# Kernel optimization log

Measured on AMD Instinct MI355X. Metric: run time of the kernel, lower is better.

## Reference

```python
import jax, jax.numpy as jnp
import numpy as np

DIM = 512
N_HEADS = 8
HEAD_DIM = DIM // N_HEADS


def rope_pos(T, head_dim, dtype=jnp.float32):
    inv_freq = 1.0 / (10000.0 ** (jnp.arange(0, head_dim, 2, dtype=jnp.float32) / head_dim))
    t = jnp.arange(T, dtype=jnp.float32)
    freqs = jnp.einsum('i,j->ij', t, inv_freq)            # [T, head_dim/2]
    return jnp.concatenate([freqs, freqs], axis=-1).astype(dtype)  # [T, head_dim]


def rotate_half(x):
    x1, x2 = jnp.split(x, 2, axis=-1)
    return jnp.concatenate([-x2, x1], axis=-1)


def apply_rope(pos, t):
    # pos: [T, hd] -> broadcast to [1,1,T,hd]; t: [B,H,T,hd]
    pos = pos[None, None, :, :]
    return t * jnp.cos(pos) + rotate_half(t) * jnp.sin(pos)


def setup_inputs() -> dict:
    key = jax.random.key(0)
    ks = jax.random.split(key, 6)
    B, T = 4, 2048
    x = jax.random.normal(ks[0], (B, T, DIM), dtype=jnp.float32)
    mask = jnp.zeros((B, T), dtype=jnp.float32)  # additive mask
    s = 1.0 / np.sqrt(DIM)
    qkv_w = jax.random.normal(ks[1], (3 * DIM, DIM), dtype=jnp.float32) * s
    qkv_b = jnp.zeros((3 * DIM,), dtype=jnp.float32)
    proj_w = jax.random.normal(ks[2], (DIM, DIM), dtype=jnp.float32) * s
    proj_b = jnp.zeros((DIM,), dtype=jnp.float32)
    return {"x": x, "mask": mask, "qkv_w": qkv_w, "qkv_b": qkv_b,
            "proj_w": proj_w, "proj_b": proj_b}


def reference(x, mask, qkv_w, qkv_b, proj_w, proj_b):
    B, T, C = x.shape
    qkv = x @ qkv_w.T + qkv_b                       # [B,T,3C]
    qkv = qkv.reshape(B, T, 3, N_HEADS, HEAD_DIM)
    q, k, v = qkv[:, :, 0], qkv[:, :, 1], qkv[:, :, 2]  # [B,T,H,hd]
    q = q.transpose(0, 2, 1, 3)                     # [B,H,T,hd]
    k = k.transpose(0, 2, 1, 3)
    v = v.transpose(0, 2, 1, 3)
    pos = rope_pos(T, HEAD_DIM, x.dtype)
    q = apply_rope(pos, q)
    k = apply_rope(pos, k)
    scores = jnp.einsum('bhqd,bhkd->bhqk', q, k) * (1.0 / np.sqrt(HEAD_DIM))
    scores = scores + mask[:, None, None, :]        # 2D mask -> [B,1,1,T]
    probs = jax.nn.softmax(scores.astype(jnp.float32), axis=-1).astype(x.dtype)
    # dropout is identity in eval mode
    out = jnp.einsum('bhqk,bhkd->bhqd', probs, v)   # [B,H,T,hd]
    out = out.transpose(0, 2, 1, 3).reshape(B, T, C)
    return out @ proj_w.T + proj_b
```

## Files before the change

### kernel.cpp

```cpp
#include <hip/hip_runtime.h>
#include <math.h>


typedef __attribute__((ext_vector_type(8))) short bf16x8;
typedef __attribute__((ext_vector_type(4))) float floatx4;

#define LOG2E 1.44269504088896f

__device__ __forceinline__ unsigned short f2bf(float f) {
  unsigned int u = __float_as_uint(f);
  u += 0x7fffu + ((u >> 16) & 1u);
  return (unsigned short)(u >> 16);
}

__device__ __forceinline__ unsigned int cvtpk_bf16(float a, float b) {
  unsigned int r;
  asm("v_cvt_pk_bf16_f32 %0, %1, %2" : "=v"(r) : "v"(a), "v"(b));
  return r;
}

__device__ __forceinline__ void gld_lds16(unsigned short* lds, const unsigned short* g) {
  __builtin_amdgcn_global_load_lds(
      (const __attribute__((address_space(1))) unsigned int*)g,
      (__attribute__((address_space(3))) unsigned int*)lds, 16, 0, 0);
}

__global__ __launch_bounds__(256) void prep_kernel(
    const float* __restrict__ x, const float* __restrict__ wq, const float* __restrict__ wp,
    unsigned short* __restrict__ xb, unsigned short* __restrict__ wqb,
    unsigned short* __restrict__ wpb, float* __restrict__ cosT, float* __restrict__ sinT) {
  int i = blockIdx.x * 256 + threadIdx.x;
  if (i < 655360) {
    int base = i * 8;
    const float* src;
    unsigned short* dst;
    int j;
    if (base < 4194304)      { src = x;  dst = xb;  j = base; }
    else if (base < 4980736) { src = wq; dst = wqb; j = base - 4194304; }
    else                     { src = wp; dst = wpb; j = base - 4980736; }
    float4 a = *(const float4*)(src + j);
    float4 b = *(const float4*)(src + j + 4);
    uint4 r;
    r.x = cvtpk_bf16(a.x, a.y);
    r.y = cvtpk_bf16(a.z, a.w);
    r.z = cvtpk_bf16(b.x, b.y);
    r.w = cvtpk_bf16(b.z, b.w);
    *(uint4*)(dst + j) = r;
  } else if (i < 720896) {
    int j = i - 655360;
    int t = j >> 5, f = j & 31;
    double fr = (double)t * pow(10000.0, -(double)f / 32.0);
    cosT[j] = (float)cos(fr);
    sinT[j] = (float)sin(fr);
  }
}

__global__ __launch_bounds__(256) void qkv_kernel(
    const unsigned short* __restrict__ xb, const unsigned short* __restrict__ wqb,
    const float* __restrict__ qkv_b, const float* __restrict__ cosT,
    const float* __restrict__ sinT, unsigned short* __restrict__ Qb,
    unsigned short* __restrict__ Kb, unsigned short* __restrict__ Vtb) {
  __shared__ __align__(16) unsigned short As[2][128 * 32];
  __shared__ __align__(16) unsigned short Bs[2][128 * 32];
  const int tid = threadIdx.x;
  const int wave = tid >> 6, lane = tid & 63, ln = lane & 15, quad = lane >> 4;
  const int m0 = blockIdx.x * 128, n0 = blockIdx.y * 128;
  const int wr = (wave >> 1) * 64, wc = (wave & 1) * 64;

  floatx4 acc[4][4];
#pragma unroll
  for (int i = 0; i < 4; ++i)
#pragma unroll
    for (int j = 0; j < 4; ++j) acc[i][j] = (floatx4){0.f, 0.f, 0.f, 0.f};

  const int c0 = tid, c1 = tid + 256;
  const int ar0 = c0 >> 2, ak0 = (c0 & 3) * 8;
  const int ar1 = c1 >> 2, ak1 = (c1 & 3) * 8;

  gld_lds16(As[0] + c0 * 8, xb + (size_t)(m0 + ar0) * 512 + ak0);
  gld_lds16(As[0] + c1 * 8, xb + (size_t)(m0 + ar1) * 512 + ak1);
  gld_lds16(Bs[0] + c0 * 8, wqb + (size_t)(n0 + ar0) * 512 + ak0);
  gld_lds16(Bs[0] + c1 * 8, wqb + (size_t)(n0 + ar1) * 512 + ak1);
  __syncthreads();

  for (int kt = 0; kt < 16; ++kt) {
    const int cur = kt & 1;
    if (kt < 15) {
      const int kn = (kt + 1) * 32;
      gld_lds16(As[cur ^ 1] + c0 * 8, xb + (size_t)(m0 + ar0) * 512 + kn + ak0);
      gld_lds16(As[cur ^ 1] + c1 * 8, xb + (size_t)(m0 + ar1) * 512 + kn + ak1);
      gld_lds16(Bs[cur ^ 1] + c0 * 8, wqb + (size_t)(n0 + ar0) * 512 + kn + ak0);
      gld_lds16(Bs[cur ^ 1] + c1 * 8, wqb + (size_t)(n0 + ar1) * 512 + kn + ak1);
    }
    bf16x8 af[4], bfb[4];
#pragma unroll
    for (int mi = 0; mi < 4; ++mi)
      af[mi] = *(const bf16x8*)(As[cur] + (wr + mi * 16 + ln) * 32 + quad * 8);
#pragma unroll
    for (int ni = 0; ni < 4; ++ni)
      bfb[ni] = *(const bf16x8*)(Bs[cur] + (wc + ni * 16 + ln) * 32 + quad * 8);
#pragma unroll
    for (int mi = 0; mi < 4; ++mi)
#pragma unroll
      for (int ni = 0; ni < 4; ++ni)
        acc[mi][ni] = __builtin_amdgcn_mfma_f32_16x16x32_bf16(af[mi], bfb[ni], acc[mi][ni], 0, 0, 0);
    __syncthreads();
  }

  const int colbase = n0 + wc;
  const int mat = colbase >> 9;
  const int h = (colbase & 511) >> 6;
  float bias[4];
#pragma unroll
  for (int ni = 0; ni < 4; ++ni) bias[ni] = qkv_b[colbase + ni * 16 + ln];

  if (mat == 2) {
#pragma unroll
    for (int mi = 0; mi < 4; ++mi) {
      int row0 = m0 + wr + mi * 16 + quad * 4;
      int bidx = row0 >> 11, t = row0 & 2047;
#pragma unroll
      for (int ni = 0; ni < 4; ++ni) {
        int d = ni * 16 + ln;
        ushort4 pk;
        pk.x = f2bf(acc[mi][ni][0] + bias[ni]);
        pk.y = f2bf(acc[mi][ni][1] + bias[ni]);
        pk.z = f2bf(acc[mi][ni][2] + bias[ni]);
        pk.w = f2bf(acc[mi][ni][3] + bias[ni]);
        *(ushort4*)(Vtb + ((size_t)(bidx * 8 + h) * 64 + d) * 2048 + t) = pk;
      }
    }
  } else {
    unsigned short* dst = (mat == 0) ? Qb : Kb;
    const float sc = (mat == 0) ? 0.125f * LOG2E : 1.0f;
#pragma unroll
    for (int mi = 0; mi < 4; ++mi) {
#pragma unroll
      for (int r = 0; r < 4; ++r) {
        int row = m0 + wr + mi * 16 + quad * 4 + r;
        int bidx = row >> 11, t = row & 2047;
        const float* cr = cosT + t * 32;
        const float* sr = sinT + t * 32;
        size_t obase = ((size_t)(bidx * 8 + h) * 2048 + t) * 64;
#pragma unroll
        for (int ni = 0; ni < 2; ++ni) {
          int dlo = ni * 16 + ln;
          float cv = cr[dlo], sv = sr[dlo];
          float xlo = acc[mi][ni][r] + bias[ni];
          float xhi = acc[mi][ni + 2][r] + bias[ni + 2];
          dst[obase + dlo]      = f2bf((xlo * cv - xhi * sv) * sc);
          dst[obase + dlo + 32] = f2bf((xhi * cv + xlo * sv) * sc);
        }
      }
    }
  }
}

__global__ __launch_bounds__(512) void attn_kernel(
    const unsigned short* __restrict__ Qb, const unsigned short* __restrict__ Kb,
    const unsigned short* __restrict__ Vtb, const float* __restrict__ mask,
    unsigned short* __restrict__ attnb) {
  __shared__ __align__(16) unsigned short Ks[64 * 64];
  __shared__ __align__(16) unsigned short Vs[64 * 64];
  __shared__ __align__(16) unsigned short Ps[128 * 64];

  const int tid = threadIdx.x;
  const int wave = tid >> 6, lane = tid & 63, ln = lane & 15, quad = lane >> 4;
  const int swz = (ln & 7) << 3;
  const int bh = blockIdx.y;
  const int b = bh >> 3, h = bh & 7;
  const int q0 = blockIdx.x * 128;
  const int wq = wave * 16;

  const unsigned short* Qhead = Qb + (size_t)bh * 2048 * 64;
  const unsigned short* Khead = Kb + (size_t)bh * 2048 * 64;
  const unsigned short* Vhead = Vtb + (size_t)bh * 64 * 2048;

  bf16x8 qf[2];
#pragma unroll
  for (int ks = 0; ks < 2; ++ks)
    qf[ks] = *(const bf16x8*)(Qhead + (size_t)(q0 + wq + ln) * 64 + ks * 32 + quad * 8);

  floatx4 o[4];
#pragma unroll
  for (int mi2 = 0; mi2 < 4; ++mi2) o[mi2] = (floatx4){0.f, 0.f, 0.f, 0.f};
  float mrun = -INFINITY;
  float lrun = 0.f;

  const int srow = tid >> 3;
  const int scol = (tid & 7) * 8;
  const int sdst = srow * 64 + (scol ^ ((srow & 7) << 3));
  uint4 kpre = *(const uint4*)(Khead + (size_t)srow * 64 + scol);
  uint4 vpre = *(const uint4*)(Vhead + (size_t)srow * 2048 + scol);

  for (int k0 = 0; k0 < 2048; k0 += 64) {
    __syncthreads();
    *(uint4*)(Ks + sdst) = kpre;
    *(uint4*)(Vs + sdst) = vpre;
    __syncthreads();
    if (k0 + 64 < 2048) {
      kpre = *(const uint4*)(Khead + (size_t)(k0 + 64 + srow) * 64 + scol);
      vpre = *(const uint4*)(Vhead + (size_t)srow * 2048 + k0 + 64 + scol);
    }

    floatx4 sm[4];
#pragma unroll
    for (int mi = 0; mi < 4; ++mi) {
      bf16x8 kf0 = *(const bf16x8*)(Ks + (mi * 16 + ln) * 64 + ((quad * 8) ^ swz));
      bf16x8 kf1 = *(const bf16x8*)(Ks + (mi * 16 + ln) * 64 + ((32 + quad * 8) ^ swz));
      floatx4 a = (floatx4){0.f, 0.f, 0.f, 0.f};
      a = __builtin_amdgcn_mfma_f32_16x16x32_bf16(kf0, qf[0], a, 0, 0, 0);
      a = __builtin_amdgcn_mfma_f32_16x16x32_bf16(kf1, qf[1], a, 0, 0, 0);
      sm[mi] = a;
    }
#pragma unroll
    for (int mi = 0; mi < 4; ++mi) {
      float4 mv = *(const float4*)(mask + b * 2048 + k0 + mi * 16 + quad * 4);
      sm[mi][0] += mv.x * LOG2E; sm[mi][1] += mv.y * LOG2E;
      sm[mi][2] += mv.z * LOG2E; sm[mi][3] += mv.w * LOG2E;
    }
    float vmax = fmaxf(fmaxf(sm[0][0], sm[0][1]), fmaxf(sm[0][2], sm[0][3]));
#pragma unroll
    for (int mi = 1; mi < 4; ++mi)
      vmax = fmaxf(vmax, fmaxf(fmaxf(sm[mi][0], sm[mi][1]), fmaxf(sm[mi][2], sm[mi][3])));
    vmax = fmaxf(vmax, __shfl_xor(vmax, 16));
    vmax = fmaxf(vmax, __shfl_xor(vmax, 32));
    if (__any(vmax > mrun)) {
      float nm = fmaxf(mrun, vmax);
      float alpha = exp2f(mrun - nm);
      mrun = nm;
      lrun *= alpha;
#pragma unroll
      for (int mi2 = 0; mi2 < 4; ++mi2) {
        o[mi2][0] *= alpha; o[mi2][1] *= alpha;
        o[mi2][2] *= alpha; o[mi2][3] *= alpha;
      }
    }
    float psum = 0.f;
#pragma unroll
    for (int mi = 0; mi < 4; ++mi)
#pragma unroll
      for (int r = 0; r < 4; ++r) {
        float p = exp2f(sm[mi][r] - mrun);
        sm[mi][r] = p;
        psum += p;
      }
    psum += __shfl_xor(psum, 16);
    psum += __shfl_xor(psum, 32);
    lrun += psum;

#pragma unroll
    for (int mi = 0; mi < 4; ++mi) {
      uint2 pk;
      pk.x = cvtpk_bf16(sm[mi][0], sm[mi][1]);
      pk.y = cvtpk_bf16(sm[mi][2], sm[mi][3]);
      *(uint2*)(Ps + (wq + ln) * 64 + ((mi * 16 + quad * 4) ^ swz)) = pk;
    }
#pragma unroll
    for (int ks = 0; ks < 2; ++ks) {
      bf16x8 pb = *(const bf16x8*)(Ps + (wq + ln) * 64 + ((ks * 32 + quad * 8) ^ swz));
#pragma unroll
      for (int mi2 = 0; mi2 < 4; ++mi2) {
        bf16x8 vf = *(const bf16x8*)(Vs + (mi2 * 16 + ln) * 64 + ((ks * 32 + quad * 8) ^ swz));
        o[mi2] = __builtin_amdgcn_mfma_f32_16x16x32_bf16(vf, pb, o[mi2], 0, 0, 0);
      }
    }
  }

  {
    float inv = 1.f / lrun;
    int t = q0 + wq + ln;
    size_t base = ((size_t)b * 2048 + t) * 512 + h * 64;
#pragma unroll
    for (int mi2 = 0; mi2 < 4; ++mi2) {
      uint2 pk;
      pk.x = cvtpk_bf16(o[mi2][0] * inv, o[mi2][1] * inv);
      pk.y = cvtpk_bf16(o[mi2][2] * inv, o[mi2][3] * inv);
      *(uint2*)(attnb + base + mi2 * 16 + quad * 4) = pk;
    }
  }
}

__global__ __launch_bounds__(512) void proj_kernel(
    const unsigned short* __restrict__ ab, const unsigned short* __restrict__ wpb,
    const float* __restrict__ proj_b, float* __restrict__ out) {
  __shared__ __align__(16) unsigned short As[2][128 * 32];
  __shared__ __align__(16) unsigned short Bs[2][128 * 32];
  const int tid = threadIdx.x;
  const int wave = tid >> 6, lane = tid & 63, ln = lane & 15, quad = lane >> 4;
  const int m0 = blockIdx.x * 128, n0 = blockIdx.y * 128;
  const int wr = (wave >> 1) * 32, wc = (wave & 1) * 64;

  floatx4 acc[2][4];
#pragma unroll
  for (int i = 0; i < 2; ++i)
#pragma unroll
    for (int j = 0; j < 4; ++j) acc[i][j] = (floatx4){0.f, 0.f, 0.f, 0.f};

  const int ar = tid >> 2, ak = (tid & 3) * 8;

  gld_lds16(As[0] + tid * 8, ab + (size_t)(m0 + ar) * 512 + ak);
  gld_lds16(Bs[0] + tid * 8, wpb + (size_t)(n0 + ar) * 512 + ak);
  __syncthreads();

  for (int kt = 0; kt < 16; ++kt) {
    const int cur = kt & 1;
    if (kt < 15) {
      const int kn = (kt + 1) * 32;
      gld_lds16(As[cur ^ 1] + tid * 8, ab + (size_t)(m0 + ar) * 512 + kn + ak);
      gld_lds16(Bs[cur ^ 1] + tid * 8, wpb + (size_t)(n0 + ar) * 512 + kn + ak);
    }
    bf16x8 af[2], bfb[4];
#pragma unroll
    for (int mi = 0; mi < 2; ++mi)
      af[mi] = *(const bf16x8*)(As[cur] + (wr + mi * 16 + ln) * 32 + quad * 8);
#pragma unroll
    for (int ni = 0; ni < 4; ++ni)
      bfb[ni] = *(const bf16x8*)(Bs[cur] + (wc + ni * 16 + ln) * 32 + quad * 8);
#pragma unroll
    for (int mi = 0; mi < 2; ++mi)
#pragma unroll
      for (int ni = 0; ni < 4; ++ni)
        acc[mi][ni] = __builtin_amdgcn_mfma_f32_16x16x32_bf16(af[mi], bfb[ni], acc[mi][ni], 0, 0, 0);
    __syncthreads();
  }

#pragma unroll
  for (int mi = 0; mi < 2; ++mi)
#pragma unroll
    for (int ni = 0; ni < 4; ++ni) {
      int col = n0 + wc + ni * 16 + ln;
      float pb = proj_b[col];
#pragma unroll
      for (int r = 0; r < 4; ++r) {
        int row = m0 + wr + mi * 16 + quad * 4 + r;
        out[(size_t)row * 512 + col] = acc[mi][ni][r] + pb;
      }
    }
}

extern "C" void kernel_launch(void* const* d_in, const int* in_sizes, int n_in,
                              void* d_out, int out_size, void* d_ws, size_t ws_size,
                              hipStream_t stream) {
  const float* x      = (const float*)d_in[0];
  const float* mask   = (const float*)d_in[1];
  const float* qkv_w  = (const float*)d_in[2];
  const float* qkv_b  = (const float*)d_in[3];
  const float* proj_w = (const float*)d_in[4];
  const float* proj_b = (const float*)d_in[5];
  float* out = (float*)d_out;

  char* ws = (char*)d_ws;
  unsigned short* xb   = (unsigned short*)(ws);
  unsigned short* wqb  = (unsigned short*)(ws + 8388608);
  unsigned short* wpb  = (unsigned short*)(ws + 9961472);
  float* cosT          = (float*)(ws + 10485760);
  float* sinT          = (float*)(ws + 10747904);
  unsigned short* Qb   = (unsigned short*)(ws + 11010048);
  unsigned short* Kb   = (unsigned short*)(ws + 19398656);
  unsigned short* Vtb  = (unsigned short*)(ws + 27787264);
  unsigned short* attnb= (unsigned short*)(ws + 36175872);

  prep_kernel<<<2816, 256, 0, stream>>>(x, qkv_w, proj_w, xb, wqb, wpb, cosT, sinT);
  dim3 g1(64, 12);
  qkv_kernel<<<g1, 256, 0, stream>>>(xb, wqb, qkv_b, cosT, sinT, Qb, Kb, Vtb);
  dim3 g2(16, 32);
  attn_kernel<<<g2, 512, 0, stream>>>(Qb, Kb, Vtb, mask, attnb);
  dim3 g3(64, 4);
  proj_kernel<<<g3, 512, 0, stream>>>(attnb, wpb, proj_b, out);
}
```

Before: 196.8 us.

## Double-buffer K/V tiles in attention and stage V transpose through LDS

New measurement: 185.7 us. -5.7%, faster.

```diff
diff --git a/kernel.cpp b/kernel.cpp
--- a/kernel.cpp
+++ b/kernel.cpp
@@ -60,8 +60,7 @@
     const float* __restrict__ qkv_b, const float* __restrict__ cosT,
     const float* __restrict__ sinT, unsigned short* __restrict__ Qb,
     unsigned short* __restrict__ Kb, unsigned short* __restrict__ Vtb) {
-  __shared__ __align__(16) unsigned short As[2][128 * 32];
-  __shared__ __align__(16) unsigned short Bs[2][128 * 32];
+  __shared__ __align__(16) unsigned short SM[2][2][128 * 32];
   const int tid = threadIdx.x;
   const int wave = tid >> 6, lane = tid & 63, ln = lane & 15, quad = lane >> 4;
   const int m0 = blockIdx.x * 128, n0 = blockIdx.y * 128;
@@ -77,28 +76,28 @@
   const int ar0 = c0 >> 2, ak0 = (c0 & 3) * 8;
   const int ar1 = c1 >> 2, ak1 = (c1 & 3) * 8;
 
-  gld_lds16(As[0] + c0 * 8, xb + (size_t)(m0 + ar0) * 512 + ak0);
-  gld_lds16(As[0] + c1 * 8, xb + (size_t)(m0 + ar1) * 512 + ak1);
-  gld_lds16(Bs[0] + c0 * 8, wqb + (size_t)(n0 + ar0) * 512 + ak0);
-  gld_lds16(Bs[0] + c1 * 8, wqb + (size_t)(n0 + ar1) * 512 + ak1);
+  gld_lds16(SM[0][0] + c0 * 8, xb + (size_t)(m0 + ar0) * 512 + ak0);
+  gld_lds16(SM[0][0] + c1 * 8, xb + (size_t)(m0 + ar1) * 512 + ak1);
+  gld_lds16(SM[0][1] + c0 * 8, wqb + (size_t)(n0 + ar0) * 512 + ak0);
+  gld_lds16(SM[0][1] + c1 * 8, wqb + (size_t)(n0 + ar1) * 512 + ak1);
   __syncthreads();
 
   for (int kt = 0; kt < 16; ++kt) {
     const int cur = kt & 1;
     if (kt < 15) {
       const int kn = (kt + 1) * 32;
-      gld_lds16(As[cur ^ 1] + c0 * 8, xb + (size_t)(m0 + ar0) * 512 + kn + ak0);
-      gld_lds16(As[cur ^ 1] + c1 * 8, xb + (size_t)(m0 + ar1) * 512 + kn + ak1);
-      gld_lds16(Bs[cur ^ 1] + c0 * 8, wqb + (size_t)(n0 + ar0) * 512 + kn + ak0);
-      gld_lds16(Bs[cur ^ 1] + c1 * 8, wqb + (size_t)(n0 + ar1) * 512 + kn + ak1);
+      gld_lds16(SM[cur ^ 1][0] + c0 * 8, xb + (size_t)(m0 + ar0) * 512 + kn + ak0);
+      gld_lds16(SM[cur ^ 1][0] + c1 * 8, xb + (size_t)(m0 + ar1) * 512 + kn + ak1);
+      gld_lds16(SM[cur ^ 1][1] + c0 * 8, wqb + (size_t)(n0 + ar0) * 512 + kn + ak0);
+      gld_lds16(SM[cur ^ 1][1] + c1 * 8, wqb + (size_t)(n0 + ar1) * 512 + kn + ak1);
     }
     bf16x8 af[4], bfb[4];
 #pragma unroll
     for (int mi = 0; mi < 4; ++mi)
-      af[mi] = *(const bf16x8*)(As[cur] + (wr + mi * 16 + ln) * 32 + quad * 8);
+      af[mi] = *(const bf16x8*)(SM[cur][0] + (wr + mi * 16 + ln) * 32 + quad * 8);
 #pragma unroll
     for (int ni = 0; ni < 4; ++ni)
-      bfb[ni] = *(const bf16x8*)(Bs[cur] + (wc + ni * 16 + ln) * 32 + quad * 8);
+      bfb[ni] = *(const bf16x8*)(SM[cur][1] + (wc + ni * 16 + ln) * 32 + quad * 8);
 #pragma unroll
     for (int mi = 0; mi < 4; ++mi)
 #pragma unroll
@@ -109,28 +108,41 @@
 
   const int colbase = n0 + wc;
   const int mat = colbase >> 9;
-  const int h = (colbase & 511) >> 6;
   float bias[4];
 #pragma unroll
   for (int ni = 0; ni < 4; ++ni) bias[ni] = qkv_b[colbase + ni * 16 + ln];
 
   if (mat == 2) {
-#pragma unroll
-    for (int mi = 0; mi < 4; ++mi) {
-      int row0 = m0 + wr + mi * 16 + quad * 4;
-      int bidx = row0 >> 11, t = row0 & 2047;
+    unsigned short* Ts = &SM[0][0][0];
+#pragma unroll
+    for (int mi = 0; mi < 4; ++mi) {
+      int r0 = wr + mi * 16 + quad * 4;
 #pragma unroll
       for (int ni = 0; ni < 4; ++ni) {
-        int d = ni * 16 + ln;
+        int c = wc + ni * 16 + ln;
         ushort4 pk;
         pk.x = f2bf(acc[mi][ni][0] + bias[ni]);
         pk.y = f2bf(acc[mi][ni][1] + bias[ni]);
         pk.z = f2bf(acc[mi][ni][2] + bias[ni]);
         pk.w = f2bf(acc[mi][ni][3] + bias[ni]);
-        *(ushort4*)(Vtb + ((size_t)(bidx * 8 + h) * 64 + d) * 2048 + t) = pk;
-      }
+        *(ushort4*)(Ts + c * 128 + (r0 ^ ((c & 7) << 3))) = pk;
+      }
+    }
+    __syncthreads();
+    const int d2 = tid >> 1, seg = tid & 1;
+    const int h0 = (n0 & 511) >> 6;
+    const int hh = d2 >> 6, dd = d2 & 63;
+    const int bidx = m0 >> 11, tl0 = m0 & 2047;
+    unsigned short* dst = Vtb + ((size_t)(bidx * 8 + h0 + hh) * 64 + dd) * 2048 + tl0;
+    const int xr = (d2 & 7) << 3;
+#pragma unroll
+    for (int j = 0; j < 8; ++j) {
+      int g = seg * 64 + j * 8;
+      uint4 v = *(const uint4*)(Ts + d2 * 128 + (g ^ xr));
+      *(uint4*)(dst + g) = v;
     }
   } else {
+    const int h = (colbase & 511) >> 6;
     unsigned short* dst = (mat == 0) ? Qb : Kb;
     const float sc = (mat == 0) ? 0.125f * LOG2E : 1.0f;
 #pragma unroll
@@ -160,8 +172,8 @@
     const unsigned short* __restrict__ Qb, const unsigned short* __restrict__ Kb,
     const unsigned short* __restrict__ Vtb, const float* __restrict__ mask,
     unsigned short* __restrict__ attnb) {
-  __shared__ __align__(16) unsigned short Ks[64 * 64];
-  __shared__ __align__(16) unsigned short Vs[64 * 64];
+  __shared__ __align__(16) unsigned short Ks[2][64 * 64];
+  __shared__ __align__(16) unsigned short Vs[2][64 * 64];
   __shared__ __align__(16) unsigned short Ps[128 * 64];
 
   const int tid = threadIdx.x;
@@ -190,15 +202,20 @@
   const int srow = tid >> 3;
   const int scol = (tid & 7) * 8;
   const int sdst = srow * 64 + (scol ^ ((srow & 7) << 3));
-  uint4 kpre = *(const uint4*)(Khead + (size_t)srow * 64 + scol);
-  uint4 vpre = *(const uint4*)(Vhead + (size_t)srow * 2048 + scol);
-
-  for (int k0 = 0; k0 < 2048; k0 += 64) {
-    __syncthreads();
-    *(uint4*)(Ks + sdst) = kpre;
-    *(uint4*)(Vs + sdst) = vpre;
-    __syncthreads();
-    if (k0 + 64 < 2048) {
+
+  {
+    uint4 k0v = *(const uint4*)(Khead + (size_t)srow * 64 + scol);
+    uint4 v0v = *(const uint4*)(Vhead + (size_t)srow * 2048 + scol);
+    *(uint4*)(Ks[0] + sdst) = k0v;
+    *(uint4*)(Vs[0] + sdst) = v0v;
+  }
+  __syncthreads();
+
+  for (int kt = 0; kt < 32; ++kt) {
+    const int cur = kt & 1;
+    const int k0 = kt * 64;
+    uint4 kpre, vpre;
+    if (kt < 31) {
       kpre = *(const uint4*)(Khead + (size_t)(k0 + 64 + srow) * 64 + scol);
       vpre = *(const uint4*)(Vhead + (size_t)srow * 2048 + k0 + 64 + scol);
     }
@@ -206,8 +223,8 @@
     floatx4 sm[4];
 #pragma unroll
     for (int mi = 0; mi < 4; ++mi) {
-      bf16x8 kf0 = *(const bf16x8*)(Ks + (mi * 16 + ln) * 64 + ((quad * 8) ^ swz));
-      bf16x8 kf1 = *(const bf16x8*)(Ks + (mi * 16 + ln) * 64 + ((32 + quad * 8) ^ swz));
+      bf16x8 kf0 = *(const bf16x8*)(Ks[cur] + (mi * 16 + ln) * 64 + ((quad * 8) ^ swz));
+      bf16x8 kf1 = *(const bf16x8*)(Ks[cur] + (mi * 16 + ln) * 64 + ((32 + quad * 8) ^ swz));
       floatx4 a = (floatx4){0.f, 0.f, 0.f, 0.f};
       a = __builtin_amdgcn_mfma_f32_16x16x32_bf16(kf0, qf[0], a, 0, 0, 0);
       a = __builtin_amdgcn_mfma_f32_16x16x32_bf16(kf1, qf[1], a, 0, 0, 0);
@@ -261,9 +278,15 @@
       bf16x8 pb = *(const bf16x8*)(Ps + (wq + ln) * 64 + ((ks * 32 + quad * 8) ^ swz));
 #pragma unroll
       for (int mi2 = 0; mi2 < 4; ++mi2) {
-        bf16x8 vf = *(const bf16x8*)(Vs + (mi2 * 16 + ln) * 64 + ((ks * 32 + quad * 8) ^ swz));
+        bf16x8 vf = *(const bf16x8*)(Vs[cur] + (mi2 * 16 + ln) * 64 + ((ks * 32 + quad * 8) ^ swz));
         o[mi2] = __builtin_amdgcn_mfma_f32_16x16x32_bf16(vf, pb, o[mi2], 0, 0, 0);
       }
+    }
+
+    if (kt < 31) {
+      *(uint4*)(Ks[cur ^ 1] + sdst) = kpre;
+      *(uint4*)(Vs[cur ^ 1] + sdst) = vpre;
+      __syncthreads();
     }
   }
 
```
